# Kernel tuning notes

Measured on AMD Instinct MI355X. Metric: run time of the kernel, lower is better.

## Reference

```python
import jax, jax.numpy as jnp
import numpy as np
import math

D_MODEL = 1024
N_HEAD = 16
HEAD_DIM = D_MODEL // N_HEAD
D_FF = 4096
NUM_STEPS = 100.0
RESCALE = 4000.0
EPS = 1e-5


def _sin_emb(t):
    # SinusoidalPosEmb: t scaled by rescale_steps/num_steps
    half = D_MODEL // 2
    x = t.astype(jnp.float32) / NUM_STEPS * RESCALE
    freqs = jnp.exp(jnp.arange(half, dtype=jnp.float32) * (-math.log(10000.0) / (half - 1)))
    e = x[:, None] * freqs[None, :]
    return jnp.concatenate([jnp.sin(e), jnp.cos(e)], axis=-1)


def _ln(x):
    m = jnp.mean(x, axis=-1, keepdims=True)
    v = jnp.var(x, axis=-1, keepdims=True)
    return (x - m) / jnp.sqrt(v + EPS)


def _gelu2(x):
    return x * jax.nn.sigmoid(1.702 * x)


def setup_inputs() -> dict:
    key = jax.random.key(0)
    ks = jax.random.split(key, 24)
    B, S, D, F = 4, 512, D_MODEL, D_FF
    std = 0.02
    inp = {
        'src': jax.random.normal(ks[0], (B, S, D), dtype=jnp.float32),
        'src_mask': jax.random.randint(ks[1], (B, 1, S, S), 0, 2).astype(bool),
        'timestep': jax.random.randint(ks[2], (B,), 0, 100, dtype=jnp.int32),
        'attention_bias': jax.random.normal(ks[3], (B, N_HEAD, S, S), dtype=jnp.float32),
        # AdaLayerNorm linear: D -> 2D (scale, shift)
        'W_ada': jax.random.normal(ks[4], (D, 2 * D), dtype=jnp.float32) * std,
        'b_ada': jnp.zeros((2 * D,), dtype=jnp.float32),
        'Wq': jax.random.normal(ks[5], (D, D), dtype=jnp.float32) * std,
        'bq': jnp.zeros((D,), dtype=jnp.float32),
        'Wk': jax.random.normal(ks[6], (D, D), dtype=jnp.float32) * std,
        'bk': jnp.zeros((D,), dtype=jnp.float32),
        'Wv': jax.random.normal(ks[7], (D, D), dtype=jnp.float32) * std,
        'bv': jnp.zeros((D,), dtype=jnp.float32),
        'Wo': jax.random.normal(ks[8], (D, D), dtype=jnp.float32) * std,
        'bo': jnp.zeros((D,), dtype=jnp.float32),
        'W1': jax.random.normal(ks[9], (D, F), dtype=jnp.float32) * std,
        'b1': jnp.zeros((F,), dtype=jnp.float32),
        'W2': jax.random.normal(ks[10], (F, D), dtype=jnp.float32) * std,
        'b2': jnp.zeros((D,), dtype=jnp.float32),
        'g2': jnp.ones((D,), dtype=jnp.float32),
        'beta2': jnp.zeros((D,), dtype=jnp.float32),
    }
    return inp


def reference(src, src_mask, timestep, attention_bias, W_ada, b_ada,
              Wq, bq, Wk, bk, Wv, bv, Wo, bo, W1, b1, W2, b2, g2, beta2):
    B, S, D = src.shape
    # AdaLayerNorm: LN(x) * (1 + scale) + shift, scale/shift from timestep emb
    emb = jax.nn.silu(_sin_emb(timestep)) @ W_ada + b_ada  # [B, 2D]
    scale, shift = jnp.split(emb[:, None, :], 2, axis=-1)  # each [B,1,D]
    x = _ln(src) * (1.0 + scale) + shift

    # Self-attention with spatial bias + fp32 masked softmax
    q = (x @ Wq + bq).reshape(B, S, N_HEAD, HEAD_DIM).transpose(0, 2, 1, 3)
    k = (x @ Wk + bk).reshape(B, S, N_HEAD, HEAD_DIM).transpose(0, 2, 1, 3)
    v = (x @ Wv + bv).reshape(B, S, N_HEAD, HEAD_DIM).transpose(0, 2, 1, 3)
    scores = jnp.einsum('bhqd,bhkd->bhqk', q / math.sqrt(HEAD_DIM), k)
    scores = scores + attention_bias
    scores = jnp.where(src_mask, -jnp.inf, scores.astype(jnp.float32))
    probs = jax.nn.softmax(scores, axis=-1).astype(v.dtype)
    ctx = jnp.einsum('bhqk,bhkd->bhqd', probs, v)
    ctx = ctx.transpose(0, 2, 1, 3).reshape(B, S, D)
    x = x + (ctx @ Wo + bo)  # residual from AdaLN output (as in source)

    # FFN with gelu2 on LN2(x)
    h = _ln(x) * g2 + beta2
    ff = _gelu2(h @ W1 + b1) @ W2 + b2
    return x + ff
```

## Files before the change

kernel.cpp:

```cpp
#include <hip/hip_runtime.h>
#include <math.h>

typedef __bf16 bf16x8 __attribute__((ext_vector_type(8)));
typedef float  f32x4  __attribute__((ext_vector_type(4)));
typedef unsigned short u16x8 __attribute__((ext_vector_type(8)));

__device__ __forceinline__ float bf2f(unsigned short u) {
    return __uint_as_float(((unsigned int)u) << 16);
}
__device__ __forceinline__ unsigned short f2bf_n(float f) {
    return __builtin_bit_cast(unsigned short, (__bf16)f);
}
__device__ __forceinline__ void gl_lds16(const unsigned short* g, unsigned short* l) {
    __builtin_amdgcn_global_load_lds(
        (const __attribute__((address_space(1))) unsigned int*)g,
        (__attribute__((address_space(3))) unsigned int*)l, 16, 0, 0);
}

#define BATCH 4
#define SEQ 512
#define DM 1024
#define NH 16
#define DH 64
#define DFF 4096
#define MROWS (BATCH * SEQ)

__global__ __launch_bounds__(256) void fill0_kernel(float* __restrict__ out) {
    out[blockIdx.x * 256 + threadIdx.x] = 0.0f;
}

__global__ __launch_bounds__(256) void tconv_kernel(const float* __restrict__ in,
                                                    unsigned short* __restrict__ out,
                                                    int K, int N) {
    __shared__ float tile[64][33];
    const int n0 = blockIdx.x * 32, k0 = blockIdx.y * 64;
    const int t = threadIdx.x;
    const int tx = t & 31, ty = t >> 5;
    #pragma unroll
    for (int i = 0; i < 8; ++i)
        tile[ty + i * 8][tx] = in[(size_t)(k0 + ty + i * 8) * N + n0 + tx];
    __syncthreads();
    const int nr = t >> 3;
    const int ks = (t & 7) * 8;
    u16x8 v;
    #pragma unroll
    for (int j = 0; j < 8; ++j) v[j] = f2bf_n(tile[ks + j][nr]);
    *(u16x8*)&out[(size_t)(n0 + nr) * K + k0 + ks] = v;
}

__global__ __launch_bounds__(256) void tconv4_kernel(const float* __restrict__ i0,
                                                     const float* __restrict__ i1,
                                                     const float* __restrict__ i2,
                                                     const float* __restrict__ i3,
                                                     unsigned short* __restrict__ o0,
                                                     unsigned short* __restrict__ o1,
                                                     unsigned short* __restrict__ o2,
                                                     unsigned short* __restrict__ o3) {
    const int z = blockIdx.z;
    const float* in = (z == 0) ? i0 : (z == 1) ? i1 : (z == 2) ? i2 : i3;
    unsigned short* out = (z == 0) ? o0 : (z == 1) ? o1 : (z == 2) ? o2 : o3;
    __shared__ float tile[64][33];
    const int n0 = blockIdx.x * 32, k0 = blockIdx.y * 64;
    const int t = threadIdx.x;
    const int tx = t & 31, ty = t >> 5;
    #pragma unroll
    for (int i = 0; i < 8; ++i)
        tile[ty + i * 8][tx] = in[(size_t)(k0 + ty + i * 8) * 1024 + n0 + tx];
    __syncthreads();
    const int nr = t >> 3;
    const int ks = (t & 7) * 8;
    u16x8 v;
    #pragma unroll
    for (int j = 0; j < 8; ++j) v[j] = f2bf_n(tile[ks + j][nr]);
    *(u16x8*)&out[(size_t)(n0 + nr) * 1024 + k0 + ks] = v;
}

__global__ void semb_kernel(const int* __restrict__ ts, float* __restrict__ semb) {
    int b = blockIdx.x;
    float x = (float)ts[b] * 40.0f;
    for (int j = threadIdx.x; j < 1024; j += 256) {
        int idx = (j < 512) ? j : (j - 512);
        float fr = expf(-9.210340371976184f * (float)idx / 511.0f);
        float e = x * fr;
        float v = (j < 512) ? sinf(e) : cosf(e);
        semb[b * 1024 + j] = v / (1.0f + expf(-v));
    }
}

__global__ __launch_bounds__(256) void ada_part_kernel(const float* __restrict__ semb,
                                                       const float* __restrict__ W,
                                                       float* __restrict__ part) {
    const int nb = blockIdx.x, kc = blockIdx.y;
    const int t = threadIdx.x;
    __shared__ float e_s[4][64];
    e_s[t >> 6][t & 63] = semb[(t >> 6) * 1024 + kc * 64 + (t & 63)];
    __syncthreads();
    const int n = nb * 128 + (t & 127);
    const int half = t >> 7;
    float a0 = 0.f, a1 = 0.f, a2 = 0.f, a3 = 0.f;
    const int kk0 = half * 32;
    #pragma unroll 8
    for (int kk = kk0; kk < kk0 + 32; ++kk) {
        const float w = W[(size_t)(kc * 64 + kk) * 2048 + n];
        a0 += e_s[0][kk] * w; a1 += e_s[1][kk] * w;
        a2 += e_s[2][kk] * w; a3 += e_s[3][kk] * w;
    }
    const int j = kc * 2 + half;
    float* p = part + (size_t)j * 4 * 2048 + n;
    p[0] = a0; p[2048] = a1; p[2 * 2048] = a2; p[3 * 2048] = a3;
}

__global__ __launch_bounds__(256) void ada_red_kernel(const float* __restrict__ part,
                                                      const float* __restrict__ bias,
                                                      float* __restrict__ ss) {
    const int idx = blockIdx.x * 256 + threadIdx.x;
    const int b = idx >> 11, n = idx & 2047;
    float acc = bias[n];
    #pragma unroll 8
    for (int j = 0; j < 32; ++j) acc += part[((size_t)j * 4 + b) * 2048 + n];
    ss[b * 2048 + n] = acc;
}

__global__ __launch_bounds__(256) void adaln_kernel(const float* __restrict__ src,
                                                    const float* __restrict__ ss,
                                                    unsigned short* __restrict__ xb) {
    int r = blockIdx.x;
    int b = r >> 9;
    int t = threadIdx.x;
    float4 v4 = *reinterpret_cast<const float4*>(&src[(size_t)r * DM + t * 4]);
    float v[4] = {v4.x, v4.y, v4.z, v4.w};
    float s = v[0] + v[1] + v[2] + v[3];
    float q = v[0]*v[0] + v[1]*v[1] + v[2]*v[2] + v[3]*v[3];
    #pragma unroll
    for (int off = 32; off > 0; off >>= 1) { s += __shfl_down(s, off); q += __shfl_down(q, off); }
    __shared__ float red[8];
    if ((t & 63) == 0) { red[t >> 6] = s; red[4 + (t >> 6)] = q; }
    __syncthreads();
    s = red[0] + red[1] + red[2] + red[3];
    q = red[4] + red[5] + red[6] + red[7];
    float mean = s * (1.0f / DM);
    float var = q * (1.0f / DM) - mean * mean;
    float rstd = rsqrtf(var + 1e-5f);
    ushort4 o;
    o.x = f2bf_n((v[0]-mean)*rstd*(1.0f+ss[b*2048 + t*4+0]) + ss[b*2048+1024 + t*4+0]);
    o.y = f2bf_n((v[1]-mean)*rstd*(1.0f+ss[b*2048 + t*4+1]) + ss[b*2048+1024 + t*4+1]);
    o.z = f2bf_n((v[2]-mean)*rstd*(1.0f+ss[b*2048 + t*4+2]) + ss[b*2048+1024 + t*4+2]);
    o.w = f2bf_n((v[3]-mean)*rstd*(1.0f+ss[b*2048 + t*4+3]) + ss[b*2048+1024 + t*4+3]);
    *reinterpret_cast<ushort4*>(&xb[(size_t)r * DM + t * 4]) = o;
}

__global__ __launch_bounds__(256) void ln2_kernel(const unsigned short* __restrict__ x,
                                                  const float* __restrict__ g2,
                                                  const float* __restrict__ beta2,
                                                  unsigned short* __restrict__ hout) {
    int r = blockIdx.x;
    int t = threadIdx.x;
    ushort4 s4 = *reinterpret_cast<const ushort4*>(&x[(size_t)r * DM + t * 4]);
    float v[4] = {bf2f(s4.x), bf2f(s4.y), bf2f(s4.z), bf2f(s4.w)};
    float s = v[0] + v[1] + v[2] + v[3];
    float q = v[0]*v[0] + v[1]*v[1] + v[2]*v[2] + v[3]*v[3];
    #pragma unroll
    for (int off = 32; off > 0; off >>= 1) { s += __shfl_down(s, off); q += __shfl_down(q, off); }
    __shared__ float red[8];
    if ((t & 63) == 0) { red[t >> 6] = s; red[4 + (t >> 6)] = q; }
    __syncthreads();
    s = red[0] + red[1] + red[2] + red[3];
    q = red[4] + red[5] + red[6] + red[7];
    float mean = s * (1.0f / DM);
    float var = q * (1.0f / DM) - mean * mean;
    float rstd = rsqrtf(var + 1e-5f);
    ushort4 o;
    o.x = f2bf_n((v[0]-mean)*rstd*g2[t*4+0] + beta2[t*4+0]);
    o.y = f2bf_n((v[1]-mean)*rstd*g2[t*4+1] + beta2[t*4+1]);
    o.z = f2bf_n((v[2]-mean)*rstd*g2[t*4+2] + beta2[t*4+2]);
    o.w = f2bf_n((v[3]-mean)*rstd*g2[t*4+3] + beta2[t*4+3]);
    *reinterpret_cast<ushort4*>(&hout[(size_t)r * DM + t * 4]) = o;
}

template<int MODE, int TN>
__global__ __launch_bounds__(256) void gemm_gl(
    const unsigned short* __restrict__ A,
    const unsigned short* __restrict__ Wta, const unsigned short* __restrict__ Wtb,
    const unsigned short* __restrict__ Wtc,
    const float* __restrict__ ba, const float* __restrict__ bbb, const float* __restrict__ bc,
    const unsigned short* __restrict__ resid,
    unsigned short* __restrict__ oa, unsigned short* __restrict__ ob,
    unsigned short* __restrict__ oc,
    float* __restrict__ outF,
    int M, int N, int K, int ldk)
{
    constexpr int CR  = 128 + TN;
    constexpr int RPW = CR / 4;
    constexpr int NI  = RPW / 8;
    constexpr int WAVE_N = (TN == 128) ? 2 : 1;
    constexpr int WAVE_M = 4 / WAVE_N;
    constexpr int AM = 128 / (WAVE_M * 16);
    constexpr int AN = TN / (WAVE_N * 16);

    __shared__ unsigned short LDSu[CR * 64];

    const int gx = gridDim.x, gy = gridDim.y;
    const int nwg = gx * gy * gridDim.z;
    const int wid = blockIdx.x + gx * (blockIdx.y + gy * blockIdx.z);
    const int aid = (wid & 7) * (nwg >> 3) + (wid >> 3);
    const int plane = gx * gy;
    const int sel = aid / plane;
    const int pid = aid % plane;
    const int by = pid % gy;
    const int bx = pid / gy;

    const unsigned short* Wt = (sel == 0) ? Wta : (sel == 1) ? Wtb : Wtc;
    const float* bias = (sel == 0) ? ba : (sel == 1) ? bbb : bc;
    unsigned short* outB = (sel == 0) ? oa : (sel == 1) ? ob : oc;

    const int t = threadIdx.x;
    const int lane = t & 63;
    const int w = t >> 6;
    const int l15 = lane & 15, l4 = lane >> 4;
    const int wm = w / WAVE_N, wn = w % WAVE_N;
    const int m0 = by * 128, n0 = bx * TN;

    f32x4 acc[AM][AN];
    #pragma unroll
    for (int i = 0; i < AM; ++i)
        #pragma unroll
        for (int j = 0; j < AN; ++j)
            #pragma unroll
            for (int r = 0; r < 4; ++r) acc[i][j][r] = 0.0f;

    const int gg = (lane & 7) ^ (lane >> 3);
    const unsigned short* gp[NI];
    unsigned short* lp[NI];
    #pragma unroll
    for (int i = 0; i < NI; ++i) {
        const int cr = w * RPW + i * 8 + (lane >> 3);
        gp[i] = (cr < 128) ? (A + (size_t)(m0 + cr) * K + gg * 8)
                           : (Wt + (size_t)(n0 + cr - 128) * ldk + gg * 8);
        lp[i] = LDSu + (w * RPW + i * 8) * 64;
    }

    const int NT = K / 64;
    for (int kt = 0; kt < NT; ++kt) {
        const int k0 = kt * 64;
        #pragma unroll
        for (int i = 0; i < NI; ++i) gl_lds16(gp[i] + k0, lp[i]);
        __syncthreads();

        #pragma unroll
        for (int kk = 0; kk < 2; ++kk) {
            const int slot = ((kk * 4 + l4) ^ (l15 & 7)) * 8;
            bf16x8 af[AM], bfr[AN];
            #pragma unroll
            for (int mt = 0; mt < AM; ++mt) {
                const int row = wm * (AM * 16) + mt * 16 + l15;
                u16x8 tmp = *(const u16x8*)(LDSu + row * 64 + slot);
                af[mt] = __builtin_bit_cast(bf16x8, tmp);
            }
            #pragma unroll
            for (int nt = 0; nt < AN; ++nt) {
                const int row = 128 + wn * (AN * 16) + nt * 16 + l15;
                u16x8 tmp = *(const u16x8*)(LDSu + row * 64 + slot);
                bfr[nt] = __builtin_bit_cast(bf16x8, tmp);
            }
            #pragma unroll
            for (int mt = 0; mt < AM; ++mt)
                #pragma unroll
                for (int nt = 0; nt < AN; ++nt)
                    acc[mt][nt] = __builtin_amdgcn_mfma_f32_16x16x32_bf16(
                        af[mt], bfr[nt], acc[mt][nt], 0, 0, 0);
        }
        if (kt + 1 < NT) __syncthreads();
    }

    #pragma unroll
    for (int mt = 0; mt < AM; ++mt) {
        const int mbase = m0 + wm * (AM * 16) + mt * 16 + l4 * 4;
        #pragma unroll
        for (int nt = 0; nt < AN; ++nt) {
            const int n = n0 + wn * (AN * 16) + nt * 16 + l15;
            const float bs = bias[n];
            #pragma unroll
            for (int r = 0; r < 4; ++r) {
                const int m = mbase + r;
                float v = acc[mt][nt][r] + bs;
                if (MODE == 2) v = v / (1.0f + expf(-1.702f * v));
                if (MODE == 1 || MODE == 3) v += bf2f(resid[(size_t)m * N + n]);
                if (MODE == 3) outF[(size_t)m * N + n] = v;
                else           outB[(size_t)m * N + n] = f2bf_n(v);
            }
        }
    }
}

#define QB2 32
#define AKT 64
#define KROW 72
#define VROW 72
#define PROW 72
#define SBPIT 72

__global__ __launch_bounds__(128) void attn_mfma(const unsigned short* __restrict__ qbuf,
                                                 const unsigned short* __restrict__ kbuf,
                                                 const unsigned short* __restrict__ vbuf,
                                                 const float* __restrict__ attb,
                                                 const int* __restrict__ mask,
                                                 unsigned short* __restrict__ ctx) {
    __shared__ unsigned short Ks[AKT * KROW];
    __shared__ unsigned short Vt[DH * VROW];
    __shared__ unsigned short Pb[2 * 16 * PROW];
    __shared__ unsigned short Sb[QB2 * SBPIT];
    const int t = threadIdx.x;
    const int lane = t & 63;
    const int w = t >> 6;
    const int l15 = lane & 15, l4 = lane >> 4;
    const int q0 = blockIdx.x * QB2;
    const int h = blockIdx.y;
    const int b = blockIdx.z;

    bf16x8 qf[2];
    {
        const unsigned short* qrow = qbuf + ((size_t)(b * SEQ + q0 + w * 16 + l15)) * DM + h * DH;
        u16x8 t0 = *(const u16x8*)(qrow + l4 * 8);
        u16x8 t1 = *(const u16x8*)(qrow + 32 + l4 * 8);
        qf[0] = __builtin_bit_cast(bf16x8, t0);
        qf[1] = __builtin_bit_cast(bf16x8, t1);
    }

    float m[4] = {-1e30f, -1e30f, -1e30f, -1e30f};
    float l[4] = {0.0f, 0.0f, 0.0f, 0.0f};
    f32x4 o[4];
    #pragma unroll
    for (int dt = 0; dt < 4; ++dt)
        #pragma unroll
        for (int r = 0; r < 4; ++r) o[dt][r] = 0.0f;

    unsigned short* Pw = Pb + w * 16 * PROW;

    const int kr = t >> 1, c0 = (t & 1) * 32;
    const int kp = t & 31, vg = t >> 5;

    u16x8 rk0, rk1, rk2, rk3, rv0, rv1, rv2, rv3;
    float4 rb[4];
    int4   rm[4];

#define LOADT(KT) {                                                                     \
    const int kbase = (KT) * AKT;                                                       \
    const unsigned short* gk = kbuf + ((size_t)(b * SEQ + kbase + kr)) * DM + h * DH + c0; \
    rk0 = *(const u16x8*)gk;        rk1 = *(const u16x8*)(gk + 8);                      \
    rk2 = *(const u16x8*)(gk + 16); rk3 = *(const u16x8*)(gk + 24);                     \
    const unsigned short* gv = vbuf + ((size_t)(b * SEQ + kbase + 2 * kp)) * DM + h * DH + vg * 8; \
    rv0 = *(const u16x8*)gv;        rv1 = *(const u16x8*)(gv + DM);                     \
    rv2 = *(const u16x8*)(gv + 32); rv3 = *(const u16x8*)(gv + DM + 32);                \
    const float* bp = attb + (((size_t)(b * NH + h)) * SEQ + (q0 + w * 16)) * SEQ + kbase; \
    const int* mp = mask + ((size_t)(b * SEQ) + q0 + w * 16) * SEQ + kbase;             \
    _Pragma("unroll")                                                                   \
    for (int i = 0; i < 4; ++i) {                                                       \
        const int e = lane + i * 64; const int row = e >> 4, cg = e & 15;               \
        rb[i] = *(const float4*)&bp[(size_t)row * SEQ + cg * 4];                        \
        rm[i] = *(const int4*)&mp[(size_t)row * SEQ + cg * 4];                          \
    } }

#define STORET() {                                                                      \
    unsigned short* s = Ks + kr * KROW + c0;                                            \
    *(u16x8*)s = rk0; *(u16x8*)(s + 8) = rk1;                                           \
    *(u16x8*)(s + 16) = rk2; *(u16x8*)(s + 24) = rk3;                                   \
    unsigned int* vt32 = (unsigned int*)Vt;                                             \
    _Pragma("unroll")                                                                   \
    for (int j = 0; j < 8; ++j) {                                                       \
        vt32[(vg * 8 + j) * (VROW / 2) + kp] =                                          \
            (unsigned int)rv0[j] | ((unsigned int)rv1[j] << 16);                        \
        vt32[((vg + 4) * 8 + j) * (VROW / 2) + kp] =                                    \
            (unsigned int)rv2[j] | ((unsigned int)rv3[j] << 16);                        \
    }                                                                                   \
    _Pragma("unroll")                                                                   \
    for (int i = 0; i < 4; ++i) {                                                       \
        const int e = lane + i * 64; const int row = e >> 4, cg = e & 15;               \
        ushort4 cc;                                                                     \
        cc.x = f2bf_n(rm[i].x ? -8e30f : 8.0f * rb[i].x);                               \
        cc.y = f2bf_n(rm[i].y ? -8e30f : 8.0f * rb[i].y);                               \
        cc.z = f2bf_n(rm[i].z ? -8e30f : 8.0f * rb[i].z);                               \
        cc.w = f2bf_n(rm[i].w ? -8e30f : 8.0f * rb[i].w);                               \
        *(ushort4*)&Sb[(w * 16 + row) * SBPIT + cg * 4] = cc;                           \
    } }

    LOADT(0);
    for (int kt = 0; kt < SEQ / AKT; ++kt) {
        __syncthreads();
        STORET();
        __syncthreads();
        if (kt + 1 < SEQ / AKT) LOADT(kt + 1);

        f32x4 acc[4];
        #pragma unroll
        for (int nt = 0; nt < 4; ++nt)
            #pragma unroll
            for (int r = 0; r < 4; ++r)
                acc[nt][r] = bf2f(Sb[(w * 16 + l4 * 4 + r) * SBPIT + nt * 16 + l15]);

        #pragma unroll
        for (int kk = 0; kk < 2; ++kk) {
            #pragma unroll
            for (int nt = 0; nt < 4; ++nt) {
                u16x8 tmp = *(const u16x8*)(Ks + (nt * 16 + l15) * KROW + kk * 32 + l4 * 8);
                acc[nt] = __builtin_amdgcn_mfma_f32_16x16x32_bf16(
                    qf[kk], __builtin_bit_cast(bf16x8, tmp), acc[nt], 0, 0, 0);
            }
        }

        float pm[4] = {-1e30f, -1e30f, -1e30f, -1e30f};
        #pragma unroll
        for (int nt = 0; nt < 4; ++nt) {
            #pragma unroll
            for (int r = 0; r < 4; ++r) {
                const float sv = acc[nt][r] * 0.125f;
                acc[nt][r] = sv;
                pm[r] = fmaxf(pm[r], sv);
            }
        }
        #pragma unroll
        for (int r = 0; r < 4; ++r) {
            #pragma unroll
            for (int off = 1; off < 16; off <<= 1)
                pm[r] = fmaxf(pm[r], __shfl_xor(pm[r], off));
        }
        float al[4], ps[4];
        #pragma unroll
        for (int r = 0; r < 4; ++r) {
            const float mn = fmaxf(m[r], pm[r]);
            al[r] = __expf(m[r] - mn);
            m[r] = mn;
            ps[r] = 0.0f;
        }
        #pragma unroll
        for (int nt = 0; nt < 4; ++nt) {
            #pragma unroll
            for (int r = 0; r < 4; ++r) {
                const float p = __expf(acc[nt][r] - m[r]);
                acc[nt][r] = p;
                ps[r] += p;
            }
        }
        #pragma unroll
        for (int r = 0; r < 4; ++r) {
            #pragma unroll
            for (int off = 1; off < 16; off <<= 1) ps[r] += __shfl_xor(ps[r], off);
            l[r] = l[r] * al[r] + ps[r];
        }
        #pragma unroll
        for (int dt = 0; dt < 4; ++dt)
            #pragma unroll
            for (int r = 0; r < 4; ++r) o[dt][r] *= al[r];

        #pragma unroll
        for (int nt = 0; nt < 4; ++nt)
            #pragma unroll
            for (int r = 0; r < 4; ++r)
                Pw[(l4 * 4 + r) * PROW + nt * 16 + l15] = f2bf_n(acc[nt][r]);

        #pragma unroll
        for (int ks = 0; ks < 2; ++ks) {
            u16x8 pa = *(const u16x8*)(Pw + l15 * PROW + ks * 32 + l4 * 8);
            #pragma unroll
            for (int dt = 0; dt < 4; ++dt) {
                u16x8 vv = *(const u16x8*)(Vt + (dt * 16 + l15) * VROW + ks * 32 + l4 * 8);
                o[dt] = __builtin_amdgcn_mfma_f32_16x16x32_bf16(
                    __builtin_bit_cast(bf16x8, pa), __builtin_bit_cast(bf16x8, vv),
                    o[dt], 0, 0, 0);
            }
        }
    }

    #pragma unroll
    for (int r = 0; r < 4; ++r) {
        const float inv = 1.0f / l[r];
        const size_t row = (size_t)(b * SEQ + q0 + w * 16 + l4 * 4 + r) * DM + h * DH;
        #pragma unroll
        for (int dt = 0; dt < 4; ++dt)
            ctx[row + dt * 16 + l15] = f2bf_n(o[dt][r] * inv);
    }
#undef LOADT
#undef STORET
}

extern "C" void kernel_launch(void* const* d_in, const int* in_sizes, int n_in,
                              void* d_out, int out_size, void* d_ws, size_t ws_size,
                              hipStream_t stream) {
    const float* src  = (const float*)d_in[0];
    const int*   mask = (const int*)d_in[1];
    const int*   ts   = (const int*)d_in[2];
    const float* attb = (const float*)d_in[3];
    const float* Wada = (const float*)d_in[4];
    const float* bada = (const float*)d_in[5];
    const float* Wq   = (const float*)d_in[6];
    const float* bq   = (const float*)d_in[7];
    const float* Wk   = (const float*)d_in[8];
    const float* bk   = (const float*)d_in[9];
    const float* Wv   = (const float*)d_in[10];
    const float* bv   = (const float*)d_in[11];
    const float* Wo   = (const float*)d_in[12];
    const float* bo   = (const float*)d_in[13];
    const float* W1   = (const float*)d_in[14];
    const float* b1   = (const float*)d_in[15];
    const float* W2   = (const float*)d_in[16];
    const float* b2   = (const float*)d_in[17];
    const float* g2   = (const float*)d_in[18];
    const float* bt2  = (const float*)d_in[19];
    float* out = (float*)d_out;

    const size_t MB = 1024 * 1024;
    const size_t NEED_FULL = 65536 + 52 * MB;
    if (ws_size < NEED_FULL) {
        fill0_kernel<<<(size_t)MROWS * DM / 256, 256, 0, stream>>>(out);
        return;
    }

    char* ws = (char*)d_ws;
    float* semb = (float*)(ws + 4096);
    float* ss   = (float*)(ws + 24576);
    char*  base = ws + 65536;
    unsigned short* slotA = (unsigned short*)(base);
    unsigned short* slotB = (unsigned short*)(base + 4 * MB);
    unsigned short* slotC = (unsigned short*)(base + 8 * MB);
    unsigned short* vb   = (unsigned short*)d_out;
    unsigned short* ctxb = (unsigned short*)((char*)d_out + 4 * MB);
    unsigned short* xb = slotA;
    unsigned short* qb = slotB;
    unsigned short* kb = slotC;
    unsigned short* x2 = slotB;
    unsigned short* hb = slotC;
    float* adap = (float*)slotC;

    unsigned short* Wtq = (unsigned short*)(base + 12 * MB);
    unsigned short* Wtk = Wtq + 1024 * 1024;
    unsigned short* Wtv = Wtk + 1024 * 1024;
    unsigned short* Wto = Wtv + 1024 * 1024;
    unsigned short* Wt1 = Wto + 1024 * 1024;
    unsigned short* Wt2 = Wt1 + (size_t)4096 * 1024;
    unsigned short* midF = (unsigned short*)(base + 36 * MB);

    tconv4_kernel<<<dim3(32, 16, 4), 256, 0, stream>>>(Wq, Wk, Wv, Wo, Wtq, Wtk, Wtv, Wto);
    tconv_kernel<<<dim3(128, 16), 256, 0, stream>>>(W1, Wt1, 1024, 4096);
    tconv_kernel<<<dim3(32, 64), 256, 0, stream>>>(W2, Wt2, 4096, 1024);

    semb_kernel<<<4, 256, 0, stream>>>(ts, semb);
    ada_part_kernel<<<dim3(16, 16), 256, 0, stream>>>(semb, Wada, adap);
    ada_red_kernel<<<32, 256, 0, stream>>>(adap, bada, ss);
    adaln_kernel<<<MROWS, 256, 0, stream>>>(src, ss, xb);

    gemm_gl<0, 128><<<dim3(8, 16, 3), 256, 0, stream>>>(
        xb, Wtq, Wtk, Wtv, bq, bk, bv, nullptr, qb, kb, vb, nullptr, MROWS, DM, DM, DM);
    attn_mfma<<<dim3(SEQ / QB2, NH, BATCH), 128, 0, stream>>>(qb, kb, vb, attb, mask, ctxb);
    gemm_gl<1, 64><<<dim3(16, 16), 256, 0, stream>>>(
        ctxb, Wto, Wto, Wto, bo, bo, bo, xb, x2, x2, x2, nullptr, MROWS, DM, DM, DM);
    ln2_kernel<<<MROWS, 256, 0, stream>>>(x2, g2, bt2, hb);
    gemm_gl<2, 128><<<dim3(32, 16), 256, 0, stream>>>(
        hb, Wt1, Wt1, Wt1, b1, b1, b1, nullptr, midF, midF, midF, nullptr, MROWS, DFF, DM, DM);
    gemm_gl<3, 64><<<dim3(16, 16), 256, 0, stream>>>(
        midF, Wt2, Wt2, Wt2, b2, b2, b2, x2, nullptr, nullptr, nullptr, out,
        MROWS, DM, DFF, DFF);
}
```

Baseline: 190.3 us.

## Split-K the final FFN down-projection into two partials plus a merge kernel

```diff
diff --git a/kernel.cpp b/kernel.cpp
--- a/kernel.cpp
+++ b/kernel.cpp
@@ -177,7 +177,26 @@
     *reinterpret_cast<ushort4*>(&hout[(size_t)r * DM + t * 4]) = o;
 }
 
-template<int MODE, int TN>
+__global__ __launch_bounds__(256) void merge_kernel(const unsigned short* __restrict__ P0,
+                                                    const unsigned short* __restrict__ P1,
+                                                    const float* __restrict__ b2,
+                                                    const unsigned short* __restrict__ x2,
+                                                    float* __restrict__ out) {
+    const size_t i4 = ((size_t)blockIdx.x * 256 + threadIdx.x) * 4;
+    const int c = (int)(i4 & 1023);
+    ushort4 p0 = *(const ushort4*)&P0[i4];
+    ushort4 p1 = *(const ushort4*)&P1[i4];
+    ushort4 xx = *(const ushort4*)&x2[i4];
+    float4 bb = *(const float4*)&b2[c];
+    float4 o;
+    o.x = bf2f(p0.x) + bf2f(p1.x) + bb.x + bf2f(xx.x);
+    o.y = bf2f(p0.y) + bf2f(p1.y) + bb.y + bf2f(xx.y);
+    o.z = bf2f(p0.z) + bf2f(p1.z) + bb.z + bf2f(xx.z);
+    o.w = bf2f(p0.w) + bf2f(p1.w) + bb.w + bf2f(xx.w);
+    *(float4*)&out[i4] = o;
+}
+
+template<int MODE, int TN, int SELMODE>
 __global__ __launch_bounds__(256) void gemm_gl(
     const unsigned short* __restrict__ A,
     const unsigned short* __restrict__ Wta, const unsigned short* __restrict__ Wtb,
@@ -187,7 +206,7 @@
     unsigned short* __restrict__ oa, unsigned short* __restrict__ ob,
     unsigned short* __restrict__ oc,
     float* __restrict__ outF,
-    int M, int N, int K, int ldk)
+    int M, int N, int K, int lda, int ldk)
 {
     constexpr int CR  = 128 + TN;
     constexpr int RPW = CR / 4;
@@ -209,9 +228,20 @@
     const int by = pid % gy;
     const int bx = pid / gy;
 
-    const unsigned short* Wt = (sel == 0) ? Wta : (sel == 1) ? Wtb : Wtc;
-    const float* bias = (sel == 0) ? ba : (sel == 1) ? bbb : bc;
-    unsigned short* outB = (sel == 0) ? oa : (sel == 1) ? ob : oc;
+    const unsigned short* Wt;
+    const float* bias;
+    unsigned short* outB;
+    int koff;
+    if (SELMODE == 0) {
+        Wt = (sel == 0) ? Wta : (sel == 1) ? Wtb : Wtc;
+        bias = (sel == 0) ? ba : (sel == 1) ? bbb : bc;
+        outB = (sel == 0) ? oa : (sel == 1) ? ob : oc;
+        koff = 0;
+    } else {
+        Wt = Wta; bias = ba;
+        outB = (sel == 0) ? oa : ob;
+        koff = sel * K;
+    }
 
     const int t = threadIdx.x;
     const int lane = t & 63;
@@ -234,8 +264,8 @@
     #pragma unroll
     for (int i = 0; i < NI; ++i) {
         const int cr = w * RPW + i * 8 + (lane >> 3);
-        gp[i] = (cr < 128) ? (A + (size_t)(m0 + cr) * K + gg * 8)
-                           : (Wt + (size_t)(n0 + cr - 128) * ldk + gg * 8);
+        gp[i] = (cr < 128) ? (A + (size_t)(m0 + cr) * lda + koff + gg * 8)
+                           : (Wt + (size_t)(n0 + cr - 128) * ldk + koff + gg * 8);
         lp[i] = LDSu + (w * RPW + i * 8) * 64;
     }
 
@@ -278,7 +308,7 @@
         #pragma unroll
         for (int nt = 0; nt < AN; ++nt) {
             const int n = n0 + wn * (AN * 16) + nt * 16 + l15;
-            const float bs = bias[n];
+            const float bs = (MODE == 5) ? 0.0f : bias[n];
             #pragma unroll
             for (int r = 0; r < 4; ++r) {
                 const int m = mbase + r;
@@ -528,6 +558,8 @@
     unsigned short* kb = slotC;
     unsigned short* x2 = slotB;
     unsigned short* hb = slotC;
+    unsigned short* P0 = slotA;
+    unsigned short* P1 = slotC;
     float* adap = (float*)slotC;
 
     unsigned short* Wtq = (unsigned short*)(base + 12 * MB);
@@ -547,15 +579,19 @@
     ada_red_kernel<<<32, 256, 0, stream>>>(adap, bada, ss);
     adaln_kernel<<<MROWS, 256, 0, stream>>>(src, ss, xb);
 
-    gemm_gl<0, 128><<<dim3(8, 16, 3), 256, 0, stream>>>(
-        xb, Wtq, Wtk, Wtv, bq, bk, bv, nullptr, qb, kb, vb, nullptr, MROWS, DM, DM, DM);
+    gemm_gl<0, 128, 0><<<dim3(8, 16, 3), 256, 0, stream>>>(
+        xb, Wtq, Wtk, Wtv, bq, bk, bv, nullptr, qb, kb, vb, nullptr,
+        MROWS, DM, DM, DM, DM);
     attn_mfma<<<dim3(SEQ / QB2, NH, BATCH), 128, 0, stream>>>(qb, kb, vb, attb, mask, ctxb);
-    gemm_gl<1, 64><<<dim3(16, 16), 256, 0, stream>>>(
-        ctxb, Wto, Wto, Wto, bo, bo, bo, xb, x2, x2, x2, nullptr, MROWS, DM, DM, DM);
+    gemm_gl<1, 64, 0><<<dim3(16, 16), 256, 0, stream>>>(
+        ctxb, Wto, Wto, Wto, bo, bo, bo, xb, x2, x2, x2, nullptr,
+        MROWS, DM, DM, DM, DM);
     ln2_kernel<<<MROWS, 256, 0, stream>>>(x2, g2, bt2, hb);
-    gemm_gl<2, 128><<<dim3(32, 16), 256, 0, stream>>>(
-        hb, Wt1, Wt1, Wt1, b1, b1, b1, nullptr, midF, midF, midF, nullptr, MROWS, DFF, DM, DM);
-    gemm_gl<3, 64><<<dim3(16, 16), 256, 0, stream>>>(
-        midF, Wt2, Wt2, Wt2, b2, b2, b2, x2, nullptr, nullptr, nullptr, out,
-        MROWS, DM, DFF, DFF);
-}
+    gemm_gl<2, 128, 0><<<dim3(32, 16), 256, 0, stream>>>(
+        hb, Wt1, Wt1, Wt1, b1, b1, b1, nullptr, midF, midF, midF, nullptr,
+        MROWS, DFF, DM, DM, DM);
+    gemm_gl<5, 128, 1><<<dim3(8, 16, 2), 256, 0, stream>>>(
+        midF, Wt2, Wt2, Wt2, b2, b2, b2, nullptr, P0, P1, nullptr, nullptr,
+        MROWS, DM, 2048, DFF, DFF);
+    merge_kernel<<<(size_t)MROWS * DM / 1024, 256, 0, stream>>>(P0, P1, b2, x2, out);
+}
```

Measured after the change: 178.3 us. 1.07x faster.
